# Kernel optimization log

Measured on AMD Instinct MI355X. Metric: run time of the kernel, lower is better.

Reference implementation:

```python
import jax, jax.numpy as jnp
import numpy as np

B, C, H, W = 4, 64, 128, 128
CQ = C // 8
EPS = 1e-5


def setup_inputs() -> dict:
    key = jax.random.key(0)
    ks = jax.random.split(key, 20)
    r = lambda k, shape, s=0.05: jax.random.normal(k, shape, dtype=jnp.float32) * s
    return {
        "x1": jax.random.normal(ks[0], (B, C, H, W), dtype=jnp.float32),
        "x2": jax.random.normal(ks[1], (B, C, H, W), dtype=jnp.float32),
        # 1x1 convs are plain channel matmuls: weight (out, in), bias (out,)
        "wqA": r(ks[2], (CQ, C)), "bqA": r(ks[3], (CQ,)),
        "wkA": r(ks[4], (CQ, C)), "bkA": r(ks[5], (CQ,)),
        "wvA": r(ks[6], (C, C)),  "bvA": r(ks[7], (C,)),
        "wqB": r(ks[8], (CQ, C)), "bqB": r(ks[9], (CQ,)),
        "wkB": r(ks[10], (CQ, C)), "bkB": r(ks[11], (CQ,)),
        "wvB": r(ks[12], (C, C)),  "bvB": r(ks[13], (C,)),
        "gA": r(ks[14], (1,), 0.1), "gB": r(ks[15], (1,), 0.1),
        "wp": r(ks[16], (C, C)), "bp": r(ks[17], (C,)),
        "bn_g": jnp.ones((C,), dtype=jnp.float32),
        "bn_b": jnp.zeros((C,), dtype=jnp.float32),
    }


def _conv1(x, w, b):
    # 1x1 conv over NCHW == per-pixel channel matmul
    return jnp.einsum('oi,bihw->bohw', w, x) + b[None, :, None, None]


def _axial(q, k, v):
    # criss-cross attention: for each pixel, attend over its row and column,
    # with the column (H) self-position masked to -inf, joint softmax over H+W.
    h = q.shape[2]
    eH = jnp.einsum('bciw,bcjw->biwj', q, k)            # [B,H,W,H] column scores
    eH = jnp.where(jnp.eye(h, dtype=bool)[:, None, :], -jnp.inf, eH)
    eW = jnp.einsum('bchi,bchj->bhij', q, k)            # [B,H,W,W] row scores
    att = jax.nn.softmax(jnp.concatenate([eH, eW], axis=3), axis=3)
    oH = jnp.einsum('bcjw,biwj->bciw', v, att[..., :h])
    oW = jnp.einsum('bchj,bhij->bchi', v, att[..., h:])
    return oH + oW


def _forward(x1, x2, wqA, bqA, wkA, bkA, wvA, bvA, wqB, bqB, wkB, bkB, wvB, bvB,
             gA, gB, wp, bp, bn_g, bn_b):
    # branch A: query from x2, key/value from x1
    out_A = _axial(_conv1(x2, wqA, bqA), _conv1(x1, wkA, bkA), _conv1(x1, wvA, bvA))
    # branch B: query/key/value all from x1
    out_B = _axial(_conv1(x1, wqB, bqB), _conv1(x1, wkB, bkB), _conv1(x1, wvB, bvB))
    diff = jnp.abs(out_A - out_B)
    p = jax.nn.gelu(_conv1(diff, wp, bp), approximate=False)
    # BatchNorm2d in training mode: batch statistics, biased variance
    m = p.mean(axis=(0, 2, 3), keepdims=True)
    v = ((p - m) ** 2).mean(axis=(0, 2, 3), keepdims=True)
    out = (p - m) / jnp.sqrt(v + EPS) * bn_g[None, :, None, None] + bn_b[None, :, None, None]
    return gA[0] * out_A + x1 + out, gB[0] * out_B + x2 + out


def reference(x1, x2, wqA, bqA, wkA, bkA, wvA, bvA, wqB, bqB, wkB, bkB, wvB, bvB,
              gA, gB, wp, bp, bn_g, bn_b):
    return _forward(x1, x2, wqA, bqA, wkA, bkA, wvA, bvA, wqB, bqB, wkB, bkB,
                    wvB, bvB, gA, gB, wp, bp, bn_g, bn_b)
```

## Files before the change

kernel.cpp:

```cpp
#include <hip/hip_runtime.h>


#define NE 4194304ull

typedef __attribute__((ext_vector_type(8))) short short8;
typedef __attribute__((ext_vector_type(4))) float f32x4;
typedef __attribute__((ext_vector_type(16))) float f32x16;

#define HD __device__ __forceinline__

HD float b2f(unsigned short u) { union { unsigned int i; float f; } v; v.i = ((unsigned int)u) << 16; return v.f; }
HD unsigned short f2b(float x) {
  union { float f; unsigned int i; } v; v.f = x;
  unsigned int r = v.i + 0x7FFFu + ((v.i >> 16) & 1u);
  return (unsigned short)(r >> 16);
}
HD unsigned int pk2(float a, float b) {
  return (unsigned int)f2b(a) | ((unsigned int)f2b(b) << 16);
}

HD float erf_fast(float x) {
  const float ax = fabsf(x);
  const float t = 1.0f / (1.0f + 0.3275911f * ax);
  const float poly = ((((1.061405429f*t - 1.453152027f)*t + 1.421413741f)*t
                       - 0.284496736f)*t + 0.254829592f)*t;
  const float y = 1.0f - poly * __expf(-ax*ax);
  return copysignf(y, x);
}

HD unsigned short ldbf(const void* s0, int i, int f) {
  return f ? f2b(((const float*)s0)[i]) : ((const unsigned short*)s0)[i];
}

__global__ __launch_bounds__(256) void prelude_kernel(
    const void* x1,
    const void* wqA, const void* bqA, const void* wkA, const void* bkA,
    const void* wvA, const void* bvA, const void* wqB, const void* bqB,
    const void* wkB, const void* bkB, const void* wvB, const void* bvB,
    const void* wp, const void* bp, const void* gA, const void* gB,
    const void* bng, const void* bnb,
    int* flag, unsigned short* wout)
{
  __shared__ int s;
  if (threadIdx.x == 0) s = 0;
  __syncthreads();
  const float a = fabsf(b2f(((const unsigned short*)x1)[threadIdx.x]));
  if (a > 1000.0f) atomicOr(&s, 1);
  __syncthreads();
  const int f = s;
  if (blockIdx.x == 0 && threadIdx.x == 0) *flag = f;

  const void* srcs[18] = {wqA,bqA,wkA,bkA,wvA,bvA,wqB,bqB,wkB,bkB,wvB,bvB,wp,bp,gA,gB,bng,bnb};
  const int   ns[18]   = {512,  8,512,  8,4096, 64,512,  8,512,  8,4096, 64,4096,64, 1, 1, 64, 64};
  unsigned short* wqkv = wout + 14696;
  float* wbias = (float*)(wout + 25960);

  const int gstride = gridDim.x * 256;
  for (int idx = blockIdx.x*256 + threadIdx.x; idx < 26136; idx += gstride) {
    if (idx < 14690) {
      int off = idx, k2 = 0;
      while (off >= ns[k2]) { off -= ns[k2]; ++k2; }
      wout[idx] = ldbf(srcs[k2], off, f);
    } else if (idx >= 25960) {
      const int i3 = idx - 25960, mt = i3 >> 4, r = i3 & 15;
      float val = 0.0f;
      if (mt == 0)      { if (r < 8) val = b2f(ldbf(bqA, r, f)); }
      else if (mt == 1) { val = b2f((r < 8) ? ldbf(bkA, r, f) : ldbf(bqB, r - 8, f)); }
      else if (mt == 2) { if (r < 8) val = b2f(ldbf(bkB, r, f)); }
      else if (mt < 7)  { val = b2f(ldbf(bvA, (mt-3)*16 + r, f)); }
      else              { val = b2f(ldbf(bvB, (mt-7)*16 + r, f)); }
      wbias[i3] = val;
    } else if (idx >= 14696) {
      const int i2 = idx - 14696;
      const int mt = i2 >> 10, rem = i2 & 1023, r = rem >> 6, ci = rem & 63;
      unsigned short val = 0;
      if (mt == 0)      { if (r < 8) val = ldbf(wqA, r*64 + ci, f); }
      else if (mt == 1) { val = (r < 8) ? ldbf(wkA, r*64 + ci, f) : ldbf(wqB, (r-8)*64 + ci, f); }
      else if (mt == 2) { if (r < 8) val = ldbf(wkB, r*64 + ci, f); }
      else if (mt < 7)  { val = ldbf(wvA, ((mt-3)*16 + r)*64 + ci, f); }
      else              { val = ldbf(wvB, ((mt-7)*16 + r)*64 + ci, f); }
      wqkv[i2] = val;
    }
  }
}

__global__ __launch_bounds__(256) void qkv_kernel(
    const void* __restrict__ x1v, const void* __restrict__ x2v, const int* __restrict__ flag,
    const unsigned short* __restrict__ wqkv, const float* __restrict__ wbias,
    unsigned short* __restrict__ q, unsigned short* __restrict__ k,
    unsigned short* __restrict__ v)
{
  const int h = blockIdx.x, b = blockIdx.y;
  const int tid = threadIdx.x, lane = tid & 63, w4 = tid >> 6;
  const int col = lane & 15, quad = lane >> 4;
  const int f32m = *flag;
  __shared__ __align__(16) char smem[16896];
  unsigned short* Xb = (unsigned short*)smem;
  unsigned short* S0 = (unsigned short*)smem;
  unsigned short* S1 = (unsigned short*)(smem + 4224);
  const size_t gb = (size_t)b*1048576 + (size_t)h*128;

  short8 Bc[2][4];
  #pragma unroll
  for (int pass = 0; pass < 2; ++pass) {
    const void* xv = pass ? x2v : x1v;
    for (int t = tid; t < 1024; t += 256) {
      const int c = t >> 4, w8 = (t & 15)*8;
      const size_t a = gb + (size_t)c*16384 + w8;
      unsigned short vals[8];
      if (f32m) {
        const float* xf = (const float*)xv;
        const float4 f0 = *(const float4*)(xf + a);
        const float4 f1 = *(const float4*)(xf + a + 4);
        vals[0]=f2b(f0.x); vals[1]=f2b(f0.y); vals[2]=f2b(f0.z); vals[3]=f2b(f0.w);
        vals[4]=f2b(f1.x); vals[5]=f2b(f1.y); vals[6]=f2b(f1.z); vals[7]=f2b(f1.w);
      } else {
        const uint4 u = *(const uint4*)((const unsigned short*)xv + a);
        vals[0]=(unsigned short)(u.x & 0xffff); vals[1]=(unsigned short)(u.x >> 16);
        vals[2]=(unsigned short)(u.y & 0xffff); vals[3]=(unsigned short)(u.y >> 16);
        vals[4]=(unsigned short)(u.z & 0xffff); vals[5]=(unsigned short)(u.z >> 16);
        vals[6]=(unsigned short)(u.w & 0xffff); vals[7]=(unsigned short)(u.w >> 16);
      }
      #pragma unroll
      for (int i = 0; i < 8; ++i) Xb[(w8 + i)*66 + c] = vals[i];
    }
    __syncthreads();
    const unsigned int* U = (const unsigned int*)Xb;
    #pragma unroll
    for (int nt2 = 0; nt2 < 2; ++nt2)
      #pragma unroll
      for (int ks = 0; ks < 2; ++ks) {
        const int n = w4*32 + nt2*16 + col;
        const int base = n*33 + (ks*32 + quad*8)/2;
        union { unsigned int u32[4]; short8 s; } p;
        #pragma unroll
        for (int jj = 0; jj < 4; ++jj) p.u32[jj] = U[base + jj];
        Bc[pass][nt2*2 + ks] = p.s;
      }
    __syncthreads();
  }

  #pragma unroll
  for (int mt = 0; mt < 11; ++mt) {
    f32x4 acc[2];
    acc[0] = (f32x4){0.f, 0.f, 0.f, 0.f};
    acc[1] = acc[0];
    #pragma unroll
    for (int ks = 0; ks < 2; ++ks) {
      union { uint4 u; short8 s; } A;
      A.u = *(const uint4*)(wqkv + mt*1024 + col*64 + ks*32 + quad*8);
      #pragma unroll
      for (int nt2 = 0; nt2 < 2; ++nt2)
        acc[nt2] = __builtin_amdgcn_mfma_f32_16x16x32_bf16(
            A.s, (mt == 0) ? Bc[1][nt2*2 + ks] : Bc[0][nt2*2 + ks], acc[nt2], 0, 0, 0);
    }
    float bias[4];
    #pragma unroll
    for (int r = 0; r < 4; ++r) bias[r] = wbias[mt*16 + quad*4 + r];
    unsigned short* S = (mt & 1) ? S1 : S0;
    #pragma unroll
    for (int nt2 = 0; nt2 < 2; ++nt2)
      #pragma unroll
      for (int r = 0; r < 4; ++r) {
        const int row = quad*4 + r;
        const int nloc = w4*32 + nt2*16 + col;
        S[row*132 + nloc] = f2b(acc[nt2][r] + bias[r]);
      }
    __syncthreads();
    if (mt < 3) {
      if (tid < 128) {
        const int nloc = tid;
        const int pixg = h*128 + nloc;
        union { unsigned short u[8]; uint4 v4; } P;
        #pragma unroll
        for (int r = 0; r < 8; ++r) P.u[r] = S[r*132 + nloc];
        if (mt == 0) {
          *(uint4*)(q + ((size_t)b*16384 + pixg)*8) = P.v4;
        } else if (mt == 1) {
          *(uint4*)(k + ((size_t)b*16384 + pixg)*8) = P.v4;
          #pragma unroll
          for (int r = 0; r < 8; ++r) P.u[r] = S[(8 + r)*132 + nloc];
          *(uint4*)(q + ((size_t)(4 + b)*16384 + pixg)*8) = P.v4;
        } else {
          *(uint4*)(k + ((size_t)(4 + b)*16384 + pixg)*8) = P.v4;
        }
      }
    } else {
      const int vm = (mt >= 7) ? mt - 7 : mt - 3;
      const int z  = (mt >= 7) ? 4 + b : b;
      const int cl = tid >> 4, u = tid & 15;
      const int co = vm*16 + cl;
      const uint4 a0 = *(const uint4*)&S[cl*132 + u*8];
      *(uint4*)(v + ((size_t)(z*64 + co)*16384 + (size_t)h*128 + u*8) ) = a0;
    }
  }
}

__global__ __launch_bounds__(256) void transpose_v(
    const unsigned short* __restrict__ vStd, unsigned short* __restrict__ vT)
{
  const int tile = blockIdx.x, c = blockIdx.y, z = blockIdx.z;
  const int h0 = (tile & 3) * 32, w0 = (tile >> 2) * 32;
  const size_t base = ((size_t)z*64 + c) * 16384;
  __shared__ unsigned short T[32][33];
  const int tid = threadIdx.x;
  for (int idx = tid; idx < 1024; idx += 256) {
    const int r = idx >> 5, cc = idx & 31;
    T[r][cc] = vStd[base + (size_t)(h0 + r)*128 + (w0 + cc)];
  }
  __syncthreads();
  for (int idx = tid; idx < 1024; idx += 256) {
    const int r = idx >> 5, cc = idx & 31;
    vT[base + (size_t)(w0 + r)*128 + (h0 + cc)] = T[cc][r];
  }
}

__global__ __launch_bounds__(256, 4) void pv_kernel(
    const unsigned short* __restrict__ q, const unsigned short* __restrict__ k,
    const unsigned short* __restrict__ vStd, const unsigned short* __restrict__ vT,
    unsigned short* __restrict__ outBrH, unsigned short* __restrict__ oColH,
    float* __restrict__ lRow, float* __restrict__ lCol)
{
  const int X = blockIdx.x, b = blockIdx.y;
  const int br = blockIdx.z & 1, dir = blockIdx.z >> 1;
  const int tid = threadIdx.x, lane = tid & 63, w4 = tid >> 6;
  const int lm = lane & 31, l5 = lane >> 5;
  const int z = br*4 + b;
  const size_t b4h = (size_t)z * 128;
  __shared__ __align__(16) char smem[16384];

  const unsigned short* vsrc = dir ? vStd : vT;
  const size_t vbase = ((size_t)z*64)*16384 + (size_t)X*128;
  for (int t = tid; t < 1024; t += 256) {
    const int c = t >> 4, slot = t & 15;
    const uint4 d = *(const uint4*)(vsrc + vbase + (size_t)c*16384 + slot*8);
    *(uint4*)(smem + c*256 + ((slot*16) ^ ((c & 15) << 4))) = d;
  }

  const uint4 zero4 = {0u, 0u, 0u, 0u};
  short8 qfr;
  {
    union { uint4 u; short8 s; } cv;
    uint4 a = zero4;
    if (l5 == 0) {
      const int m = w4*32 + lm;
      const size_t pix = (b4h + (dir ? X : m))*128 + (dir ? m : X);
      a = *(const uint4*)(q + pix*8);
    }
    cv.u = a; qfr = cv.s;
  }

  float lsum = 0.0f;
  unsigned int pka[4][4], pkb[4][4];
  #pragma unroll
  for (int jt = 0; jt < 4; ++jt) {
    union { uint4 u; short8 s; } kv;
    kv.u = zero4;
    if (l5 == 0) {
      const int j = jt*32 + lm;
      const size_t pix = (b4h + (dir ? X : j))*128 + (dir ? j : X);
      kv.u = *(const uint4*)(k + pix*8);
    }
    f32x16 sacc = (f32x16){0.f,0.f,0.f,0.f,0.f,0.f,0.f,0.f,
                           0.f,0.f,0.f,0.f,0.f,0.f,0.f,0.f};
    sacc = __builtin_amdgcn_mfma_f32_32x32x16_bf16(kv.s, qfr, sacc, 0, 0, 0);
    #pragma unroll
    for (int r2 = 0; r2 < 4; ++r2) {
      float pv4[4];
      #pragma unroll
      for (int e = 0; e < 4; ++e) {
        const int jl = e + 8*r2 + 4*l5;
        float p = 0.0f;
        if (dir || (jt != w4) || (jl != lm)) p = __expf(sacc[r2*4 + e]);
        lsum += p;
        pv4[e] = p;
      }
      pka[jt][r2] = pk2(pv4[0], pv4[1]);
      pkb[jt][r2] = pk2(pv4[2], pv4[3]);
    }
  }

  lsum += __shfl_xor(lsum, 32);
  if (l5 == 0) {
    float* lOut = dir ? lRow : lCol;
    lOut[((size_t)z*128 + X)*128 + w4*32 + lm] = lsum;
  }

  __syncthreads();

  f32x16 acc[2];
  acc[0] = (f32x16){0.f,0.f,0.f,0.f,0.f,0.f,0.f,0.f,0.f,0.f,0.f,0.f,0.f,0.f,0.f,0.f};
  acc[1] = acc[0];
  #pragma unroll
  for (int kb = 0; kb < 8; ++kb) {
    const int qq = kb & 1, jt = kb >> 1;
    const unsigned int ownA = l5 ? pka[jt][2*qq+1] : pka[jt][2*qq];
    const unsigned int ownB = l5 ? pkb[jt][2*qq+1] : pkb[jt][2*qq];
    const unsigned int sndA = l5 ? pka[jt][2*qq]   : pka[jt][2*qq+1];
    const unsigned int sndB = l5 ? pkb[jt][2*qq]   : pkb[jt][2*qq+1];
    const unsigned int rcvA = (unsigned int)__shfl_xor((int)sndA, 32);
    const unsigned int rcvB = (unsigned int)__shfl_xor((int)sndB, 32);
    union { unsigned int u[4]; short8 s; } t4;
    t4.u[0] = l5 ? rcvA : ownA;
    t4.u[1] = l5 ? rcvB : ownB;
    t4.u[2] = l5 ? ownA : rcvA;
    t4.u[3] = l5 ? ownB : rcvB;
    #pragma unroll
    for (int nb = 0; nb < 2; ++nb) {
      const int c = nb*32 + lm;
      union { uint4 u; short8 s; } bv;
      bv.u = *(const uint4*)(smem + c*256 + (((kb*2 + l5)*16) ^ ((c & 15) << 4)));
      acc[nb] = __builtin_amdgcn_mfma_f32_32x32x16_bf16(t4.s, bv.s, acc[nb], 0, 0, 0);
    }
  }

  __syncthreads();

  #pragma unroll
  for (int nb = 0; nb < 2; ++nb) {
    const int c = nb*32 + lm;
    #pragma unroll
    for (int r2 = 0; r2 < 4; ++r2) {
      uint2 u;
      u.x = pk2(acc[nb][r2*4+0], acc[nb][r2*4+1]);
      u.y = pk2(acc[nb][r2*4+2], acc[nb][r2*4+3]);
      const int mbyte = w4*64 + r2*16 + l5*8;
      *(uint2*)(smem + c*256 + (mbyte ^ ((c & 15) << 3))) = u;
    }
  }
  __syncthreads();

  unsigned short* dsth = dir ? outBrH : oColH;
  for (int t = tid; t < 2048; t += 256) {
    const int c = t >> 5, mc = t & 31;
    const uint2 u = *(const uint2*)(smem + c*256 + ((mc*8) ^ ((c & 15) << 3)));
    *(uint2*)(dsth + vbase + (size_t)c*16384 + mc*4) = u;
  }
}

__global__ __launch_bounds__(256) void combine_kernel(
    const unsigned short* __restrict__ oColU, const float* __restrict__ lRow,
    const float* __restrict__ lCol, unsigned short* __restrict__ outBr)
{
  const int tile = blockIdx.x, z = blockIdx.y, cg = blockIdx.z;
  const int h0 = (tile & 3) * 32, w0 = (tile >> 2) * 32, c0 = cg*8;
  const int tid = threadIdx.x;
  __shared__ float Tl[32][33];
  __shared__ __align__(16) float inv[32][36];
  __shared__ __align__(16) float T4[4][32][36];
  const size_t lzb = (size_t)z * 16384;
  {
    const int w = tid >> 3, h4 = (tid & 7)*4;
    const float4 vc = *(const float4*)(lCol + lzb + (size_t)(w0 + w)*128 + h0 + h4);
    Tl[w][h4+0] = vc.x; Tl[w][h4+1] = vc.y; Tl[w][h4+2] = vc.z; Tl[w][h4+3] = vc.w;
  }
  __syncthreads();
  {
    const int h = tid >> 3, w4 = (tid & 7)*4;
    const float4 lr = *(const float4*)(lRow + lzb + (size_t)(h0 + h)*128 + w0 + w4);
    float4 iv;
    iv.x = 1.0f / (lr.x + Tl[w4+0][h]);
    iv.y = 1.0f / (lr.y + Tl[w4+1][h]);
    iv.z = 1.0f / (lr.z + Tl[w4+2][h]);
    iv.w = 1.0f / (lr.w + Tl[w4+3][h]);
    *(float4*)&inv[h][w4] = iv;
  }
  __syncthreads();
  #pragma unroll
  for (int half = 0; half < 2; ++half) {
    for (int t = tid; t < 1024; t += 256) {
      const int ch = t >> 8, rem = t & 255, w = rem >> 3, h4 = (rem & 7)*4;
      const int c = c0 + half*4 + ch;
      const uint2 vc = *(const uint2*)(oColU + ((size_t)(z*64 + c))*16384
                                       + (size_t)(w0 + w)*128 + h0 + h4);
      float4 f;
      f.x = b2f((unsigned short)(vc.x & 0xffff)); f.y = b2f((unsigned short)(vc.x >> 16));
      f.z = b2f((unsigned short)(vc.y & 0xffff)); f.w = b2f((unsigned short)(vc.y >> 16));
      *(float4*)&T4[ch][w][h4] = f;
    }
    __syncthreads();
    for (int t = tid; t < 1024; t += 256) {
      const int ch = t >> 8, rem = t & 255, h = rem >> 3, w4 = (rem & 7)*4;
      const int c = c0 + half*4 + ch;
      const size_t off = ((size_t)(z*64 + c))*16384 + (size_t)(h0 + h)*128 + w0 + w4;
      const uint2 ov = *(const uint2*)(outBr + off);
      const float4 iv = *(const float4*)&inv[h][w4];
      float o0 = b2f((unsigned short)(ov.x & 0xffff));
      float o1 = b2f((unsigned short)(ov.x >> 16));
      float o2 = b2f((unsigned short)(ov.y & 0xffff));
      float o3 = b2f((unsigned short)(ov.y >> 16));
      o0 = (o0 + T4[ch][w4+0][h]) * iv.x;
      o1 = (o1 + T4[ch][w4+1][h]) * iv.y;
      o2 = (o2 + T4[ch][w4+2][h]) * iv.z;
      o3 = (o3 + T4[ch][w4+3][h]) * iv.w;
      uint2 u;
      u.x = (unsigned int)f2b(o0) | ((unsigned int)f2b(o1) << 16);
      u.y = (unsigned int)f2b(o2) | ((unsigned int)f2b(o3) << 16);
      *(uint2*)(outBr + off) = u;
    }
    __syncthreads();
  }
}

__global__ __launch_bounds__(256) void proj_kernel(
    const unsigned short* __restrict__ outA, const unsigned short* __restrict__ outB,
    const unsigned short* __restrict__ wp, const unsigned short* __restrict__ bp,
    unsigned short* __restrict__ pbuf, float* __restrict__ part)
{
  const int hp = blockIdx.x, b = blockIdx.y;
  const int tid = threadIdx.x, lane = tid & 63, w4 = tid >> 6;
  const int col = lane & 15, quad = lane >> 4;
  __shared__ __align__(16) char smem[17408];
  unsigned short* Xb = (unsigned short*)smem;
  float* S = (float*)smem;

  const size_t gb = (size_t)b*1048576 + (size_t)hp*64;
  for (int t = tid; t < 512; t += 256) {
    const int c = t >> 3, rem = t & 7;
    const size_t a = gb + (size_t)c*16384 + rem*8;
    const uint4 ua = *(const uint4*)(outA + a);
    const uint4 ub = *(const uint4*)(outB + a);
    const unsigned short* pa = (const unsigned short*)&ua;
    const unsigned short* pb = (const unsigned short*)&ub;
    const int n = rem*8;
    #pragma unroll
    for (int i = 0; i < 8; ++i)
      Xb[(n + i)*66 + c] = f2b(fabsf(b2f(pa[i]) - b2f(pb[i])));
  }
  __syncthreads();

  short8 Bc[8];
  const unsigned int* U = (const unsigned int*)Xb;
  #pragma unroll
  for (int nt = 0; nt < 4; ++nt)
    #pragma unroll
    for (int ks = 0; ks < 2; ++ks) {
      const int n = nt*16 + col;
      const int base = n*33 + (ks*32 + quad*8)/2;
      union { unsigned int u32[4]; short8 s; } p;
      #pragma unroll
      for (int jj = 0; jj < 4; ++jj) p.u32[jj] = U[base + jj];
      Bc[nt*2 + ks] = p.s;
    }
  __syncthreads();

  f32x4 acc[4];
  #pragma unroll
  for (int nt = 0; nt < 4; ++nt) acc[nt] = (f32x4){0.f, 0.f, 0.f, 0.f};
  #pragma unroll
  for (int ks = 0; ks < 2; ++ks) {
    union { uint4 u; short8 s; } A;
    A.u = *(const uint4*)(wp + (w4*16 + col)*64 + ks*32 + quad*8);
    #pragma unroll
    for (int nt = 0; nt < 4; ++nt)
      acc[nt] = __builtin_amdgcn_mfma_f32_16x16x32_bf16(A.s, Bc[nt*2 + ks], acc[nt], 0, 0, 0);
  }

  float sg1[4] = {0.f, 0.f, 0.f, 0.f}, sg2[4] = {0.f, 0.f, 0.f, 0.f};
  #pragma unroll
  for (int nt = 0; nt < 4; ++nt)
    #pragma unroll
    for (int r = 0; r < 4; ++r) {
      const float x = acc[nt][r] + b2f(bp[w4*16 + quad*4 + r]);
      const float g = 0.5f * x * (1.0f + erf_fast(x * 0.70710678118f));
      S[(w4*16 + quad*4 + r)*68 + nt*16 + col] = g;
      sg1[r] += g; sg2[r] += g*g;
    }
  const int slot = hp*4 + b;
  #pragma unroll
  for (int r = 0; r < 4; ++r) {
    float s1 = sg1[r], s2 = sg2[r];
    s1 += __shfl_xor(s1, 1); s1 += __shfl_xor(s1, 2);
    s1 += __shfl_xor(s1, 4); s1 += __shfl_xor(s1, 8);
    s2 += __shfl_xor(s2, 1); s2 += __shfl_xor(s2, 2);
    s2 += __shfl_xor(s2, 4); s2 += __shfl_xor(s2, 8);
    if (col == 0) {
      const int co = w4*16 + quad*4 + r;
      part[(size_t)co*1024 + slot] = s1;
      part[(size_t)(64 + co)*1024 + slot] = s2;
    }
  }
  __syncthreads();

  for (int t = tid; t < 1024; t += 256) {
    const int row = t >> 4, px4 = (t & 15)*4;
    const float* sp = &S[row*68 + px4];
    uint2 u;
    u.x = pk2(sp[0], sp[1]);
    u.y = pk2(sp[2], sp[3]);
    *(uint2*)(pbuf + (size_t)(b*64 + row)*16384 + hp*64 + px4) = u;
  }
}

__global__ __launch_bounds__(256) void reduce_kernel(
    const float* __restrict__ part, float* __restrict__ bnAcc)
{
  const int stat = blockIdx.x, tid = threadIdx.x;
  const float4 v = *(const float4*)(part + (size_t)stat*1024 + tid*4);
  float s = v.x + v.y + v.z + v.w;
  #pragma unroll
  for (int off = 32; off >= 1; off >>= 1) s += __shfl_xor(s, off);
  __shared__ float ws4[4];
  if ((tid & 63) == 0) ws4[tid >> 6] = s;
  __syncthreads();
  if (tid == 0) bnAcc[stat] = ws4[0] + ws4[1] + ws4[2] + ws4[3];
}

__global__ __launch_bounds__(256) void final_kernel(
    const unsigned short* __restrict__ pbuf,
    const unsigned short* __restrict__ outAH, const unsigned short* __restrict__ outBH,
    const void* __restrict__ x1v, const void* __restrict__ x2v, const int* __restrict__ flag,
    const unsigned short* __restrict__ gA, const unsigned short* __restrict__ gB,
    const unsigned short* __restrict__ bng, const unsigned short* __restrict__ bnb,
    const float* __restrict__ bnAcc, void* __restrict__ outv)
{
  const int f32m = *flag;
  const int idx = (blockIdx.x * 256 + threadIdx.x) * 4;
  const int c = (idx >> 14) & 63;
  const float invN = 1.0f / 65536.0f;
  const float s1 = bnAcc[c], s2 = bnAcc[64 + c];
  const float mean = s1 * invN;
  const float var = s2 * invN - mean*mean;
  const float scale = rsqrtf(var + 1e-5f) * b2f(bng[c]);
  const float beta = b2f(bnb[c]);
  const float ga = b2f(gA[0]), gb = b2f(gB[0]);
  const uint2 uP = *(const uint2*)(pbuf + idx);
  const uint2 uA = *(const uint2*)(outAH + idx);
  const uint2 uB = *(const uint2*)(outBH + idx);
  float p[4] = { b2f((unsigned short)(uP.x & 0xffff)), b2f((unsigned short)(uP.x >> 16)),
                 b2f((unsigned short)(uP.y & 0xffff)), b2f((unsigned short)(uP.y >> 16)) };
  float a[4] = { b2f((unsigned short)(uA.x & 0xffff)), b2f((unsigned short)(uA.x >> 16)),
                 b2f((unsigned short)(uA.y & 0xffff)), b2f((unsigned short)(uA.y >> 16)) };
  float bb[4] = { b2f((unsigned short)(uB.x & 0xffff)), b2f((unsigned short)(uB.x >> 16)),
                  b2f((unsigned short)(uB.y & 0xffff)), b2f((unsigned short)(uB.y >> 16)) };
  float xa[4], xb[4];
  if (f32m) {
    const float4 t1 = *(const float4*)((const float*)x1v + idx);
    const float4 t2 = *(const float4*)((const float*)x2v + idx);
    xa[0]=t1.x; xa[1]=t1.y; xa[2]=t1.z; xa[3]=t1.w;
    xb[0]=t2.x; xb[1]=t2.y; xb[2]=t2.z; xb[3]=t2.w;
  } else {
    const uint2 x1u = *(const uint2*)((const unsigned short*)x1v + idx);
    const uint2 x2u = *(const uint2*)((const unsigned short*)x2v + idx);
    xa[0] = b2f((unsigned short)(x1u.x & 0xffff)); xa[1] = b2f((unsigned short)(x1u.x >> 16));
    xa[2] = b2f((unsigned short)(x1u.y & 0xffff)); xa[3] = b2f((unsigned short)(x1u.y >> 16));
    xb[0] = b2f((unsigned short)(x2u.x & 0xffff)); xb[1] = b2f((unsigned short)(x2u.x >> 16));
    xb[2] = b2f((unsigned short)(x2u.y & 0xffff)); xb[3] = b2f((unsigned short)(x2u.y >> 16));
  }
  float o1f[4], o2f[4];
  #pragma unroll
  for (int t = 0; t < 4; ++t) {
    const float nv = (p[t] - mean)*scale + beta;
    o1f[t] = ga*a[t] + xa[t] + nv;
    o2f[t] = gb*bb[t] + xb[t] + nv;
  }
  if (f32m) {
    float* of = (float*)outv;
    *(float4*)(of + idx)      = (float4){o1f[0], o1f[1], o1f[2], o1f[3]};
    *(float4*)(of + NE + idx) = (float4){o2f[0], o2f[1], o2f[2], o2f[3]};
  } else {
    unsigned short* oh = (unsigned short*)outv;
    uint2 u1, u2;
    u1.x = (unsigned int)f2b(o1f[0]) | ((unsigned int)f2b(o1f[1]) << 16);
    u1.y = (unsigned int)f2b(o1f[2]) | ((unsigned int)f2b(o1f[3]) << 16);
    u2.x = (unsigned int)f2b(o2f[0]) | ((unsigned int)f2b(o2f[1]) << 16);
    u2.y = (unsigned int)f2b(o2f[2]) | ((unsigned int)f2b(o2f[3]) << 16);
    *(uint2*)(oh + idx) = u1;
    *(uint2*)(oh + NE + idx) = u2;
  }
}

extern "C" void kernel_launch(void* const* d_in, const int* in_sizes, int n_in,
                              void* d_out, int out_size, void* d_ws, size_t ws_size,
                              hipStream_t stream)
{
  const void* x1  = d_in[0];
  const void* x2  = d_in[1];

  char* ws = (char*)d_ws;
  const size_t MB = 1048576ull;
  unsigned short* q     = (unsigned short*)(ws);
  unsigned short* kk    = (unsigned short*)(ws + 2*MB);
  float* lRow           = (float*)(ws + 4*MB);
  float* lCol           = (float*)(ws + 4*MB + 512*1024);
  unsigned short* vStd  = (unsigned short*)(ws + 6*MB);
  unsigned short* vT    = (unsigned short*)(ws + 22*MB);
  unsigned short* outBrH= (unsigned short*)(ws + 38*MB);
  unsigned short* oColH = (unsigned short*)(ws + 54*MB);
  unsigned short* pbuf  = (unsigned short*)(ws + 70*MB);
  float* part           = (float*)(ws + 86*MB);
  float* bnAcc          = (float*)(ws + 102*MB);
  int*   flag           = (int*)(ws + 102*MB + 512);
  unsigned short* wC    = (unsigned short*)(ws + 102*MB + 1024);

  prelude_kernel<<<64, 256, 0, stream>>>(
      x1, d_in[2], d_in[3], d_in[4], d_in[5], d_in[6], d_in[7], d_in[8], d_in[9],
      d_in[10], d_in[11], d_in[12], d_in[13], d_in[16], d_in[17], d_in[14], d_in[15],
      d_in[18], d_in[19], flag, wC);
  qkv_kernel<<<dim3(128, 4), 256, 0, stream>>>(
      x1, x2, flag, wC + 14696, (const float*)(wC + 25960), q, kk, vStd);
  transpose_v<<<dim3(16, 64, 8), 256, 0, stream>>>(vStd, vT);
  pv_kernel<<<dim3(128, 4, 4), 256, 0, stream>>>(q, kk, vStd, vT, outBrH, oColH, lRow, lCol);
  combine_kernel<<<dim3(16, 8, 8), 256, 0, stream>>>(oColH, lRow, lCol, outBrH);
  proj_kernel<<<dim3(256, 4), 256, 0, stream>>>(outBrH, outBrH + NE, wC + 10400, wC + 14496, pbuf, part);
  reduce_kernel<<<128, 256, 0, stream>>>(part, bnAcc);
  final_kernel<<<4096, 256, 0, stream>>>(pbuf, outBrH, outBrH + NE, x1, x2, flag,
                                         wC + 14560, wC + 14561, wC + 14562, wC + 14626,
                                         bnAcc, d_out);
}
```

Before: 210.5 us.

## Process two adjacent rows/columns per pv_kernel block with interleaved phases

Each pv_kernel block now handles two adjacent X indices. It loads 256-byte contiguous V segments per channel into a doubled 32KB shared buffer, and overlaps the second score phase with the first PV phase. The grid is flattened to 1D with a swizzled block-id mapping, and the old per-phase body is split into helper functions. The aim is wider, more coalesced V loads and less per-block fixed overhead, at the cost of fewer blocks, more shared memory per block (which can lower occupancy) and more live registers.

New measurement: 219.0 us. 1.04x slower.

```diff
diff --git a/kernel.cpp b/kernel.cpp
--- a/kernel.cpp
+++ b/kernel.cpp
@@ -215,28 +215,13 @@
   }
 }
 
-__global__ __launch_bounds__(256, 4) void pv_kernel(
-    const unsigned short* __restrict__ q, const unsigned short* __restrict__ k,
-    const unsigned short* __restrict__ vStd, const unsigned short* __restrict__ vT,
-    unsigned short* __restrict__ outBrH, unsigned short* __restrict__ oColH,
-    float* __restrict__ lRow, float* __restrict__ lCol)
-{
-  const int X = blockIdx.x, b = blockIdx.y;
-  const int br = blockIdx.z & 1, dir = blockIdx.z >> 1;
-  const int tid = threadIdx.x, lane = tid & 63, w4 = tid >> 6;
-  const int lm = lane & 31, l5 = lane >> 5;
-  const int z = br*4 + b;
-  const size_t b4h = (size_t)z * 128;
-  __shared__ __align__(16) char smem[16384];
-
-  const unsigned short* vsrc = dir ? vStd : vT;
-  const size_t vbase = ((size_t)z*64)*16384 + (size_t)X*128;
-  for (int t = tid; t < 1024; t += 256) {
-    const int c = t >> 4, slot = t & 15;
-    const uint4 d = *(const uint4*)(vsrc + vbase + (size_t)c*16384 + slot*8);
-    *(uint4*)(smem + c*256 + ((slot*16) ^ ((c & 15) << 4))) = d;
-  }
-
+HD void s_phase(const unsigned short* __restrict__ q,
+                const unsigned short* __restrict__ k,
+                float* __restrict__ lOut,
+                size_t b4h, int X, int dir, int z,
+                int w4, int lm, int l5,
+                unsigned int (&pka)[4][4], unsigned int (&pkb)[4][4])
+{
   const uint4 zero4 = {0u, 0u, 0u, 0u};
   short8 qfr;
   {
@@ -249,9 +234,7 @@
     }
     cv.u = a; qfr = cv.s;
   }
-
   float lsum = 0.0f;
-  unsigned int pka[4][4], pkb[4][4];
   #pragma unroll
   for (int jt = 0; jt < 4; ++jt) {
     union { uint4 u; short8 s; } kv;
@@ -279,16 +262,14 @@
       pkb[jt][r2] = pk2(pv4[2], pv4[3]);
     }
   }
-
   lsum += __shfl_xor(lsum, 32);
-  if (l5 == 0) {
-    float* lOut = dir ? lRow : lCol;
-    lOut[((size_t)z*128 + X)*128 + w4*32 + lm] = lsum;
-  }
-
-  __syncthreads();
-
-  f32x16 acc[2];
+  if (l5 == 0) lOut[((size_t)z*128 + X)*128 + w4*32 + lm] = lsum;
+}
+
+HD void pv_phase(const char* __restrict__ Vb, int lm, int l5,
+                 const unsigned int (&pka)[4][4], const unsigned int (&pkb)[4][4],
+                 f32x16 (&acc)[2])
+{
   acc[0] = (f32x16){0.f,0.f,0.f,0.f,0.f,0.f,0.f,0.f,0.f,0.f,0.f,0.f,0.f,0.f,0.f,0.f};
   acc[1] = acc[0];
   #pragma unroll
@@ -309,13 +290,15 @@
     for (int nb = 0; nb < 2; ++nb) {
       const int c = nb*32 + lm;
       union { uint4 u; short8 s; } bv;
-      bv.u = *(const uint4*)(smem + c*256 + (((kb*2 + l5)*16) ^ ((c & 15) << 4)));
+      bv.u = *(const uint4*)(Vb + c*256 + (((kb*2 + l5)*16) ^ ((c & 15) << 4)));
       acc[nb] = __builtin_amdgcn_mfma_f32_32x32x16_bf16(t4.s, bv.s, acc[nb], 0, 0, 0);
     }
   }
-
-  __syncthreads();
-
+}
+
+HD void dst_write(char* __restrict__ Dst, const f32x16 (&acc)[2],
+                  int w4, int lm, int l5)
+{
   #pragma unroll
   for (int nb = 0; nb < 2; ++nb) {
     const int c = nb*32 + lm;
@@ -325,17 +308,74 @@
       u.x = pk2(acc[nb][r2*4+0], acc[nb][r2*4+1]);
       u.y = pk2(acc[nb][r2*4+2], acc[nb][r2*4+3]);
       const int mbyte = w4*64 + r2*16 + l5*8;
-      *(uint2*)(smem + c*256 + (mbyte ^ ((c & 15) << 3))) = u;
-    }
-  }
-  __syncthreads();
-
-  unsigned short* dsth = dir ? outBrH : oColH;
+      *(uint2*)(Dst + c*256 + (mbyte ^ ((c & 15) << 3))) = u;
+    }
+  }
+}
+
+HD void out_write(const char* __restrict__ Dst, unsigned short* __restrict__ dsth,
+                  size_t obase, int tid)
+{
   for (int t = tid; t < 2048; t += 256) {
     const int c = t >> 5, mc = t & 31;
-    const uint2 u = *(const uint2*)(smem + c*256 + ((mc*8) ^ ((c & 15) << 3)));
-    *(uint2*)(dsth + vbase + (size_t)c*16384 + mc*4) = u;
-  }
+    const uint2 u = *(const uint2*)(Dst + c*256 + ((mc*8) ^ ((c & 15) << 3)));
+    *(uint2*)(dsth + obase + (size_t)c*16384 + mc*4) = u;
+  }
+}
+
+__global__ __launch_bounds__(256, 4) void pv_kernel(
+    const unsigned short* __restrict__ q, const unsigned short* __restrict__ k,
+    const unsigned short* __restrict__ vStd, const unsigned short* __restrict__ vT,
+    unsigned short* __restrict__ outBrH, unsigned short* __restrict__ oColH,
+    float* __restrict__ lRow, float* __restrict__ lCol)
+{
+  const int id = blockIdx.x;
+  const int swz = (id & 7)*128 + (id >> 3);
+  const int Xg = swz & 63, b = (swz >> 6) & 3, zz = swz >> 8;
+  const int br = zz & 1, dir = zz >> 1;
+  const int tid = threadIdx.x, lane = tid & 63, w4 = tid >> 6;
+  const int lm = lane & 31, l5 = lane >> 5;
+  const int z = br*4 + b;
+  const size_t b4h = (size_t)z * 128;
+  const int X0 = Xg * 2;
+  __shared__ __align__(16) char smem[32768];
+
+  const unsigned short* vsrc = dir ? vStd : vT;
+  const size_t vbase0 = ((size_t)z*64)*16384 + (size_t)X0*128;
+  #pragma unroll
+  for (int it = 0; it < 8; ++it) {
+    const int t = it*256 + tid;
+    const int c = t >> 5, g = t & 31;
+    const uint4 d = *(const uint4*)(vsrc + vbase0 + (size_t)c*16384 + g*8);
+    const int xi = g >> 4, slot = g & 15;
+    *(uint4*)(smem + xi*16384 + c*256 + ((slot*16) ^ ((c & 15) << 4))) = d;
+  }
+
+  float* lOut = dir ? lRow : lCol;
+  unsigned short* dsth = dir ? outBrH : oColH;
+
+  unsigned int pkaA[4][4], pkbA[4][4];
+  s_phase(q, k, lOut, b4h, X0, dir, z, w4, lm, l5, pkaA, pkbA);
+  __syncthreads();
+
+  f32x16 acc0[2];
+  pv_phase(smem, lm, l5, pkaA, pkbA, acc0);
+
+  unsigned int pkaB[4][4], pkbB[4][4];
+  s_phase(q, k, lOut, b4h, X0 + 1, dir, z, w4, lm, l5, pkaB, pkbB);
+  __syncthreads();
+
+  dst_write(smem, acc0, w4, lm, l5);
+  __syncthreads();
+  out_write(smem, dsth, vbase0, tid);
+
+  f32x16 acc1[2];
+  pv_phase(smem + 16384, lm, l5, pkaB, pkbB, acc1);
+  __syncthreads();
+
+  dst_write(smem, acc1, w4, lm, l5);
+  __syncthreads();
+  out_write(smem, dsth, vbase0 + 128, tid);
 }
 
 __global__ __launch_bounds__(256) void combine_kernel(
@@ -600,7 +640,7 @@
   qkv_kernel<<<dim3(128, 4), 256, 0, stream>>>(
       x1, x2, flag, wC + 14696, (const float*)(wC + 25960), q, kk, vStd);
   transpose_v<<<dim3(16, 64, 8), 256, 0, stream>>>(vStd, vT);
-  pv_kernel<<<dim3(128, 4, 4), 256, 0, stream>>>(q, kk, vStd, vT, outBrH, oColH, lRow, lCol);
+  pv_kernel<<<dim3(1024), 256, 0, stream>>>(q, kk, vStd, vT, outBrH, oColH, lRow, lCol);
   combine_kernel<<<dim3(16, 8, 8), 256, 0, stream>>>(oColH, lRow, lCol, outBrH);
   proj_kernel<<<dim3(256, 4), 256, 0, stream>>>(outBrH, outBrH + NE, wC + 10400, wC + 14496, pbuf, part);
   reduce_kernel<<<128, 256, 0, stream>>>(part, bnAcc);
```
